# Optimization experiments

Hardware: AMD Instinct MI355X
Metric: run time of the kernel (lower is better)

The kernel has to match this reference:

```python
import jax, jax.numpy as jnp
import numpy as np

B, L, LQ = 64, 4096, 128
D = 32        # input_dim (value channels)
ET = 128      # embed_time
NH = 1        # num_heads
H = 128       # nhidden
NC = 6        # n_classes


def _time_emb(tt, lin_w, lin_b, per_w, per_b):
    # tt [..., T] -> [..., T, ET]; cat(Linear(1,1)(t), sin(Linear(1,ET-1)(t)))
    tt = tt[..., None]
    out1 = tt * lin_w[0, 0] + lin_b
    out2 = jnp.sin(tt @ per_w + per_b)
    return jnp.concatenate([out1, out2], axis=-1)


def _gru_dir(xs, wih, whh, bih, bhh, reverse):
    # xs [B, T, I] -> [B, T, H]; torch GRU gate math
    xs_t = jnp.swapaxes(xs, 0, 1)              # [T, B, I]
    if reverse:
        xs_t = xs_t[::-1]
    gi_all = xs_t @ wih.T + bih                # [T, B, 3H] precomputed input gates
    h0 = jnp.zeros((xs.shape[0], H), xs.dtype)

    def step(h, gi):
        gh = h @ whh.T + bhh
        ir, iz, inn = jnp.split(gi, 3, axis=-1)
        hr, hz, hn = jnp.split(gh, 3, axis=-1)
        r = jax.nn.sigmoid(ir + hr)
        z = jax.nn.sigmoid(iz + hz)
        n = jnp.tanh(inn + r * hn)
        h_new = (1.0 - z) * n + z * h
        return h_new, h_new

    _, ys = jax.lax.scan(step, h0, gi_all)     # [T, B, H]
    if reverse:
        ys = ys[::-1]
    return jnp.swapaxes(ys, 0, 1)


def _bigru(xs, wih, whh, bih, bhh):
    fwd = _gru_dir(xs, wih[0], whh[0], bih[0], bhh[0], False)
    bwd = _gru_dir(xs, wih[1], whh[1], bih[1], bhh[1], True)
    return jnp.concatenate([fwd, bwd], axis=-1)


def setup_inputs() -> dict:
    ks = jax.random.split(jax.random.key(0), 32)
    w = lambda i, s: jax.random.normal(ks[i], s, jnp.float32) * 0.05
    G3 = 3 * H
    return {
        "x": jax.random.normal(ks[0], (B, L, D), jnp.float32),
        "time_steps": jax.random.uniform(ks[1], (B, L), dtype=jnp.float32),
        "query_times": jnp.linspace(0.0, 1.0, LQ, dtype=jnp.float32),
        "lin_w": w(2, (1, 1)), "lin_b": w(3, (1,)),
        "per_w": w(4, (1, ET - 1)), "per_b": w(5, (ET - 1,)),
        "wq": w(6, (ET, ET)), "bq": w(7, (ET,)),
        "wk": w(8, (ET, ET)), "bk": w(9, (ET,)),
        "wo": w(10, (NH * D, H)), "bo": w(11, (H,)),
        "gru0_wih": w(12, (2, G3, H)), "gru0_whh": w(13, (2, G3, H)),
        "gru0_bih": w(14, (2, G3)), "gru0_bhh": w(15, (2, G3)),
        "gru1_wih": w(16, (2, G3, 2 * H)), "gru1_whh": w(17, (2, G3, H)),
        "gru1_bih": w(18, (2, G3)), "gru1_bhh": w(19, (2, G3)),
        "c1_w": w(20, (2 * H, 128)), "c1_b": w(21, (128,)),
        "c2_w": w(22, (128, 64)), "c2_b": w(23, (64,)),
        "c3_w": w(24, (64, NC)), "c3_b": w(25, (NC,)),
    }


def reference(x, time_steps, query_times, lin_w, lin_b, per_w, per_b,
              wq, bq, wk, bk, wo, bo,
              gru0_wih, gru0_whh, gru0_bih, gru0_bhh,
              gru1_wih, gru1_whh, gru1_bih, gru1_bhh,
              c1_w, c1_b, c2_w, c2_b, c3_w, c3_b):
    ek = ET // NH
    # learned time embeddings
    q = _time_emb(query_times[None, :], lin_w, lin_b, per_w, per_b)  # [1, LQ, ET]
    k = _time_emb(time_steps, lin_w, lin_b, per_w, per_b)            # [B, L, ET]
    # per-head projections
    qp = (q @ wq + bq).reshape(1, LQ, NH, ek).transpose(0, 2, 1, 3)[0]  # [NH, LQ, ek]
    kp = (k @ wk + bk).reshape(B, L, NH, ek).transpose(0, 2, 1, 3)      # [B, NH, L, ek]
    # mTAN attention: scores are channel-independent (mask=None), so the
    # per-channel repeat+softmax reduces to a single softmax over keys.
    scores = jnp.einsum('hqe,bhke->bhqk', qp, kp) / jnp.sqrt(jnp.float32(ek))
    p = jax.nn.softmax(scores, axis=-1)                                 # [B, NH, LQ, L]
    att = jnp.einsum('bhqk,bkd->bqhd', p, x).reshape(B, LQ, NH * D)
    att_out = att @ wo + bo                                             # [B, LQ, H]
    # 2-layer bidirectional GRU
    g0 = _bigru(att_out, gru0_wih, gru0_whh, gru0_bih, gru0_bhh)        # [B, LQ, 2H]
    g1 = _bigru(g0, gru1_wih, gru1_whh, gru1_bih, gru1_bhh)             # [B, LQ, 2H]
    class_in = jnp.concatenate([g1[:, -1, :H], g1[:, 0, H:]], axis=1)   # [B, 2H]
    out = ((class_in @ c1_w + c1_b) @ c2_w + c2_b) @ c3_w + c3_b        # [B, NC]
    return out
```

## Files before the change

### kernel.cpp

```cpp
#include <hip/hip_runtime.h>
#include <math.h>

#define Bn   64
#define Ln   4096
#define LQn  128
#define Dn   32
#define ETn  128
#define Hn   128
#define G3n  384
#define NDEG 12

typedef __attribute__((ext_vector_type(2))) float f32x2;

#define DPPF(x, ctrl) __int_as_float(__builtin_amdgcn_update_dpp(0, __float_as_int(x), (ctrl), 0xF, 0xF, true))
#define QP_XOR1 0xB1
#define QP_XOR2 0x4E
#define QP_B0   0x00
#define QP_B1   0x55
#define QP_B2   0xAA
#define QP_B3   0xFF

__device__ __forceinline__ float sin_poly(float x) {
    const float x2 = x * x;
    float r = -1.9841270114e-04f;
    r = fmaf(r, x2,  8.3333337680e-03f);
    r = fmaf(r, x2, -1.6666667163e-01f);
    return fmaf(r * x2, x, x);
}
__device__ __forceinline__ float cos_poly(float x) {
    const float x2 = x * x;
    float r =  2.4801587642e-05f;
    r = fmaf(r, x2, -1.3888888899e-03f);
    r = fmaf(r, x2,  4.1666667908e-02f);
    r = fmaf(r, x2, -5.0000000000e-01f);
    return fmaf(r, x2, 1.0f);
}

#define WS_C    0
#define WS_WT   4096
#define WS_B2   (WS_WT + 768*32)
#define WS_CLS  (WS_B2 + 1024)
#define WS_G0   (WS_CLS + Bn*2*Hn)
#define WS_GI   (WS_G0 + Bn*LQn*2*Hn)
#define WS_QPB  WS_G0
#define WS_BAS  (WS_G0 + 16384)
#define WS_ACCP WS_G0
#define WS_SP   (WS_G0 + 1048576)

__global__ __launch_bounds__(128) void k_basis(
    const float* __restrict__ per_w, const float* __restrict__ per_b,
    float* __restrict__ basis)
{
    const int j = threadIdx.x;
    if (j >= ETn - 1) return;
    const float w = per_w[j], b = per_b[j];
    const float sb = sin_poly(b), cb = cos_poly(b);
    float wp = 1.f;
#pragma unroll
    for (int d = 0; d < NDEG; ++d) {
        const float sd = ((d & 3) == 0) ? sb : ((d & 3) == 1) ? cb : ((d & 3) == 2) ? -sb : -cb;
        basis[d * 128 + j] = wp * sd;
        wp *= w / (float)(d + 1);
    }
}

__global__ __launch_bounds__(128) void k_qp(
    const float* __restrict__ qtimes, const float* __restrict__ lin_w,
    const float* __restrict__ lin_b, const float* __restrict__ per_w,
    const float* __restrict__ per_b, const float* __restrict__ wq,
    const float* __restrict__ bq, float* __restrict__ qp)
{
    __shared__ float qe[ETn];
    const int q = blockIdx.x, e = threadIdx.x;
    const float t = qtimes[q];
    qe[e] = (e == 0) ? fmaf(t, lin_w[0], lin_b[0])
                     : sin_poly(fmaf(t, per_w[e - 1], per_b[e - 1]));
    __syncthreads();
    float a = bq[e];
#pragma unroll 16
    for (int i = 0; i < ETn; ++i) a = fmaf(qe[i], wq[i * ETn + e], a);
    qp[q * ETn + e] = a;
}

__global__ __launch_bounds__(128) void k_qtc(
    const float* __restrict__ qp, const float* __restrict__ wk,
    const float* __restrict__ bk, const float* __restrict__ lin_w,
    const float* __restrict__ lin_b, const float* __restrict__ basis,
    float* __restrict__ C)
{
    __shared__ float qp_l[ETn], qt_l[ETn], red[96], qbk_red[32];
    const int q = blockIdx.x, tid = threadIdx.x;
    qp_l[tid] = qp[q * ETn + tid];
    __syncthreads();
    {
        const float4* wk4 = (const float4*)(wk + (size_t)tid * ETn);
        const float4* qp4 = (const float4*)qp_l;
        float a = 0.f;
#pragma unroll
        for (int k = 0; k < 32; ++k) {
            const float4 w4 = wk4[k], p4 = qp4[k];
            a += w4.x * p4.x + w4.y * p4.y + w4.z * p4.z + w4.w * p4.w;
        }
        qt_l[tid] = a;
    }
    __syncthreads();
    if (tid < 96) {
        const int d = tid >> 3, g = tid & 7;
        float p = 0.f;
        for (int j = g; j < ETn - 1; j += 8) p = fmaf(qt_l[j + 1], basis[d * 128 + j], p);
        red[tid] = p;
    } else {
        const int g2 = tid - 96;
        float p = 0.f;
#pragma unroll
        for (int k = 0; k < 4; ++k) p = fmaf(qp_l[g2 + 32 * k], bk[g2 + 32 * k], p);
        qbk_red[g2] = p;
    }
    __syncthreads();
    if (tid < NDEG) {
        const int d = tid;
        float s = red[d * 8 + 0] + red[d * 8 + 1] + red[d * 8 + 2] + red[d * 8 + 3]
                + red[d * 8 + 4] + red[d * 8 + 5] + red[d * 8 + 6] + red[d * 8 + 7];
        if (d == 0) {
            float qbk = 0.f;
#pragma unroll
            for (int k = 0; k < 32; ++k) qbk += qbk_red[k];
            s += qt_l[0] * lin_b[0] + qbk;
        }
        if (d == 1) s += qt_l[0] * lin_w[0];
        C[q * NDEG + d] = s * 0.08838834764831845f;
    }
}

__global__ __launch_bounds__(256) void k_fuse(
    const float* __restrict__ wih, const float* __restrict__ wo,
    const float* __restrict__ bo, const float* __restrict__ bih,
    float* __restrict__ Wt, float* __restrict__ bias2)
{
    const int t = blockIdx.x * 256 + threadIdx.x;
    if (t < 768 * 32) {
        const int o = t >> 5, d = t & 31;
        const float* wr = wih + (size_t)o * 128;
        const float* wc = wo + (size_t)d * 128;
        float a = 0.f;
        for (int h = 0; h < 128; ++h) a += wr[h] * wc[h];
        Wt[t] = a;
    } else if (t < 768 * 33) {
        const int o = t - 768 * 32;
        const float* wr = wih + (size_t)o * 128;
        float a = bih[o];
        for (int h = 0; h < 128; ++h) a += bo[h] * wr[h];
        bias2[o] = a;
    }
}

#define ACC8(m, pv) \
    acc[m][0].x = fmaf(pv, xa.x, acc[m][0].x); acc[m][0].y = fmaf(pv, xa.y, acc[m][0].y); \
    acc[m][0].z = fmaf(pv, xa.z, acc[m][0].z); acc[m][0].w = fmaf(pv, xa.w, acc[m][0].w); \
    acc[m][1].x = fmaf(pv, xb.x, acc[m][1].x); acc[m][1].y = fmaf(pv, xb.y, acc[m][1].y); \
    acc[m][1].z = fmaf(pv, xb.z, acc[m][1].z); acc[m][1].w = fmaf(pv, xb.w, acc[m][1].w);

__global__ __launch_bounds__(512, 2) void k_attn(
    const float* __restrict__ x, const float* __restrict__ tsteps,
    const float* __restrict__ Cc, float* __restrict__ accP, float* __restrict__ sP)
{
    __shared__ float slab[4][128][36];
    const int tid = threadIdx.x;
    const int b = blockIdx.x >> 2, lsplit = blockIdx.x & 3;
    const int i = tid & 3, qt = (tid >> 2) & 31, ls2 = tid >> 7;
    const int qown = 4 * qt + i;

    float c[NDEG];
#pragma unroll
    for (int d = 0; d < NDEG; ++d) c[d] = Cc[qown * NDEG + d];

    const int l0 = lsplit * 1024 + ls2 * 256;
    const float4* tg4 = (const float4*)(tsteps + (size_t)b * Ln + l0);
    const float4* xg  = (const float4*)(x + ((size_t)b * Ln + l0) * Dn);

    float4 acc[4][2];
#pragma unroll
    for (int m = 0; m < 4; ++m)
#pragma unroll
        for (int e = 0; e < 2; ++e) { acc[m][e].x = 0.f; acc[m][e].y = 0.f; acc[m][e].z = 0.f; acc[m][e].w = 0.f; }
    float s_own = 0.f;

    for (int k = 0; k < 64; ++k) {
        const float4 t4 = tg4[k];
#pragma unroll
        for (int jj = 0; jj < 4; ++jj) {
            const float t = (jj == 0) ? t4.x : (jj == 1) ? t4.y : (jj == 2) ? t4.z : t4.w;
            float sc = c[NDEG - 1];
#pragma unroll
            for (int d = NDEG - 2; d >= 0; --d) sc = fmaf(sc, t, c[d]);
            const float pe = __expf(sc);
            s_own += pe;
            const float p0 = DPPF(pe, QP_B0);
            const float p1 = DPPF(pe, QP_B1);
            const float p2 = DPPF(pe, QP_B2);
            const float p3 = DPPF(pe, QP_B3);
            const int lrow = (k * 4 + jj) * 8;
            const float4 xa = xg[lrow + 2 * i];
            const float4 xb = xg[lrow + 2 * i + 1];
            ACC8(0, p0) ACC8(1, p1) ACC8(2, p2) ACC8(3, p3)
        }
    }
#pragma unroll
    for (int m = 0; m < 4; ++m) {
        *(float4*)&slab[ls2][4 * qt + m][8 * i]     = acc[m][0];
        *(float4*)&slab[ls2][4 * qt + m][8 * i + 4] = acc[m][1];
    }
    slab[ls2][qown][32] = s_own;
    __syncthreads();
    const int q = tid & 127, part = tid >> 7;
#pragma unroll
    for (int j = 0; j < 2; ++j) {
        const int off = (part * 2 + j) * 4;
        float4 r  = *(float4*)&slab[0][q][off];
        float4 r1 = *(float4*)&slab[1][q][off];
        float4 r2 = *(float4*)&slab[2][q][off];
        float4 r3 = *(float4*)&slab[3][q][off];
        r.x += r1.x + r2.x + r3.x; r.y += r1.y + r2.y + r3.y;
        r.z += r1.z + r2.z + r3.z; r.w += r1.w + r2.w + r3.w;
        *(float4*)&accP[((((size_t)lsplit * Bn + b) * LQn + q) * 32) + off] = r;
    }
    if (part == 0) {
        sP[((size_t)lsplit * Bn + b) * LQn + q] =
            slab[0][q][32] + slab[1][q][32] + slab[2][q][32] + slab[3][q][32];
    }
}

__global__ __launch_bounds__(256) void k_gemm_att(
    const float* __restrict__ accP, const float* __restrict__ sP,
    const float* __restrict__ Bm, const float* __restrict__ bias,
    float* __restrict__ Cm)
{
    __shared__ float4 A_l[64 * 8];
    __shared__ float4 B_l[64 * 8];
    const int tid = threadIdx.x;
    const int m0 = blockIdx.x * 64, n0 = blockIdx.y * 64;
    const int r0 = (tid >> 4) << 2, c0 = (tid & 15) << 2;
    float acc[4][4] = {};
    const float4* Ag = (const float4*)accP;
    const float4* Bg = (const float4*)Bm;

#pragma unroll
    for (int w = 0; w < 2; ++w) {
        const int idx = tid + w * 256;
        const int row = idx >> 3, c4 = idx & 7;
        const int sc = (c4 + row + (row >> 2)) & 7;
        const int m = m0 + row;
        float4 a0 = Ag[(size_t)m * 8 + c4];
        float4 a1 = Ag[((size_t)8192  + m) * 8 + c4];
        float4 a2 = Ag[((size_t)16384 + m) * 8 + c4];
        float4 a3 = Ag[((size_t)24576 + m) * 8 + c4];
        const float inv = 1.f / (sP[m] + sP[8192 + m] + sP[16384 + m] + sP[24576 + m]);
        float4 av;
        av.x = (a0.x + a1.x + a2.x + a3.x) * inv;
        av.y = (a0.y + a1.y + a2.y + a3.y) * inv;
        av.z = (a0.z + a1.z + a2.z + a3.z) * inv;
        av.w = (a0.w + a1.w + a2.w + a3.w) * inv;
        A_l[row * 8 + sc] = av;
        B_l[row * 8 + sc] = Bg[(size_t)(n0 + row) * 8 + c4];
    }
    __syncthreads();
#pragma unroll
    for (int k4 = 0; k4 < 8; ++k4) {
        float4 av[4], bv[4];
#pragma unroll
        for (int j = 0; j < 4; ++j) {
            const int ra = r0 + j;
            av[j] = A_l[ra * 8 + ((k4 + ra + (ra >> 2)) & 7)];
        }
#pragma unroll
        for (int j = 0; j < 4; ++j) {
            const int rb = c0 + j;
            bv[j] = B_l[rb * 8 + ((k4 + rb + (rb >> 2)) & 7)];
        }
#pragma unroll
        for (int ri = 0; ri < 4; ++ri)
#pragma unroll
            for (int ci = 0; ci < 4; ++ci)
                acc[ri][ci] += av[ri].x * bv[ci].x + av[ri].y * bv[ci].y
                             + av[ri].z * bv[ci].z + av[ri].w * bv[ci].w;
    }
#pragma unroll
    for (int ri = 0; ri < 4; ++ri) {
        float4 o4;
        o4.x = acc[ri][0] + bias[n0 + c0 + 0];
        o4.y = acc[ri][1] + bias[n0 + c0 + 1];
        o4.z = acc[ri][2] + bias[n0 + c0 + 2];
        o4.w = acc[ri][3] + bias[n0 + c0 + 3];
        *(float4*)&Cm[(size_t)(m0 + r0 + ri) * 768 + n0 + c0] = o4;
    }
}

__global__ __launch_bounds__(256) void k_gemm_nt(
    const float* __restrict__ A, const float* __restrict__ Bm,
    const float* __restrict__ bias, float* __restrict__ Cm,
    int N, int K)
{
    __shared__ float4 A_l[64 * 8];
    __shared__ float4 B_l[64 * 8];
    const int tid = threadIdx.x;
    const int m0 = blockIdx.x * 64, n0 = blockIdx.y * 64;
    const int r0 = (tid >> 4) << 2, c0 = (tid & 15) << 2;
    const int K4 = K >> 2;
    float acc[4][4] = {};
    const float4* Ag = (const float4*)A;
    const float4* Bg = (const float4*)Bm;

    for (int k0 = 0; k0 < K4; k0 += 8) {
        __syncthreads();
#pragma unroll
        for (int w = 0; w < 2; ++w) {
            const int idx = tid + w * 256;
            const int row = idx >> 3, c4 = idx & 7;
            const int sc = (c4 + row + (row >> 2)) & 7;
            A_l[row * 8 + sc] = Ag[(size_t)(m0 + row) * K4 + k0 + c4];
            B_l[row * 8 + sc] = Bg[(size_t)(n0 + row) * K4 + k0 + c4];
        }
        __syncthreads();
#pragma unroll
        for (int k4 = 0; k4 < 8; ++k4) {
            float4 av[4], bv[4];
#pragma unroll
            for (int j = 0; j < 4; ++j) {
                const int ra = r0 + j;
                av[j] = A_l[ra * 8 + ((k4 + ra + (ra >> 2)) & 7)];
            }
#pragma unroll
            for (int j = 0; j < 4; ++j) {
                const int rb = c0 + j;
                bv[j] = B_l[rb * 8 + ((k4 + rb + (rb >> 2)) & 7)];
            }
#pragma unroll
            for (int ri = 0; ri < 4; ++ri)
#pragma unroll
                for (int ci = 0; ci < 4; ++ci)
                    acc[ri][ci] += av[ri].x * bv[ci].x + av[ri].y * bv[ci].y
                                 + av[ri].z * bv[ci].z + av[ri].w * bv[ci].w;
        }
    }
#pragma unroll
    for (int ri = 0; ri < 4; ++ri) {
        float4 o4;
        o4.x = acc[ri][0] + bias[n0 + c0 + 0];
        o4.y = acc[ri][1] + bias[n0 + c0 + 1];
        o4.z = acc[ri][2] + bias[n0 + c0 + 2];
        o4.w = acc[ri][3] + bias[n0 + c0 + 3];
        *(float4*)&Cm[(size_t)(m0 + r0 + ri) * N + n0 + c0] = o4;
    }
}

__global__ __launch_bounds__(256, 1) void k_gru(
    const float* __restrict__ gi, const float* __restrict__ whh,
    const float* __restrict__ bhh, float* __restrict__ seq_out,
    float* __restrict__ final_out)
{
    __shared__ float h_l[2][Hn];
    const int tid = threadIdx.x;
    const int b = blockIdx.x >> 1, dir = blockIdx.x & 1;
    const int j = tid >> 1, q = tid & 1;

    f32x2 wr[32], wz[32], wn[32];
    {
        const float* wb = whh + ((size_t)dir * G3n + j) * Hn + 64 * q;
        const f32x2* p0 = (const f32x2*)(wb);
        const f32x2* p1 = (const f32x2*)(wb + (size_t)128 * Hn);
        const f32x2* p2 = (const f32x2*)(wb + (size_t)256 * Hn);
#pragma unroll
        for (int k = 0; k < 32; ++k) { wr[k] = p0[k]; wz[k] = p1[k]; wn[k] = p2[k]; }
    }
#pragma unroll
    for (int k = 0; k < 32; ++k) {
        asm volatile("" : "+v"(wr[k]));
        asm volatile("" : "+v"(wz[k]));
        asm volatile("" : "+v"(wn[k]));
    }
    const float bhr = bhh[dir * G3n + j];
    const float bhz = bhh[dir * G3n + 128 + j];
    const float bhn = bhh[dir * G3n + 256 + j];

    if (tid < Hn) { h_l[0][tid] = 0.f; h_l[1][tid] = 0.f; }
    __syncthreads();

    const long sstride = dir ? -768 : 768;
    const float* gptr = gi + (size_t)b * LQn * 768 + dir * G3n + j
                        + (size_t)(dir ? LQn - 1 : 0) * 768;

    int cur = 0;
    float hlast = 0.f;

    auto gstep = [&](const float gir, const float giz, const float gin,
                     const int step) {
        const float hold = h_l[cur][j];
        const float4* hb = (const float4*)(&h_l[cur][q * 64]);
        f32x2 ar = {0.f, 0.f}, az = {0.f, 0.f}, an = {0.f, 0.f};
        f32x2 br = {0.f, 0.f}, bz = {0.f, 0.f}, bn = {0.f, 0.f};
#pragma unroll
        for (int cc = 0; cc < 16; ++cc) {
            float4 hv = hb[cc];
            f32x2 h01; h01.x = hv.x; h01.y = hv.y;
            f32x2 h23; h23.x = hv.z; h23.y = hv.w;
            asm("v_pk_fma_f32 %0, %1, %2, %0" : "+v"(ar) : "v"(wr[2 * cc]),     "v"(h01));
            asm("v_pk_fma_f32 %0, %1, %2, %0" : "+v"(az) : "v"(wz[2 * cc]),     "v"(h01));
            asm("v_pk_fma_f32 %0, %1, %2, %0" : "+v"(an) : "v"(wn[2 * cc]),     "v"(h01));
            asm("v_pk_fma_f32 %0, %1, %2, %0" : "+v"(br) : "v"(wr[2 * cc + 1]), "v"(h23));
            asm("v_pk_fma_f32 %0, %1, %2, %0" : "+v"(bz) : "v"(wz[2 * cc + 1]), "v"(h23));
            asm("v_pk_fma_f32 %0, %1, %2, %0" : "+v"(bn) : "v"(wn[2 * cc + 1]), "v"(h23));
        }
        float sr = (ar.x + br.x) + (ar.y + br.y);
        float sz = (az.x + bz.x) + (az.y + bz.y);
        float sn = (an.x + bn.x) + (an.y + bn.y);
        sr += DPPF(sr, QP_XOR1);
        sz += DPPF(sz, QP_XOR1);
        sn += DPPF(sn, QP_XOR1);
        const float r = 1.f / (1.f + __expf(-(gir + sr + bhr)));
        const float z = 1.f / (1.f + __expf(-(giz + sz + bhz)));
        const float nx = gin + r * (sn + bhn);
        const float n = 1.f - 2.f / (1.f + __expf(2.f * nx));
        const float hn = n + z * (hold - n);
        if (q == 0) {
            h_l[cur ^ 1][j] = hn;
            if (seq_out) {
                const int l = dir ? (LQn - 1 - step) : step;
                seq_out[((size_t)(b * LQn + l)) * (2 * Hn) + dir * Hn + j] = hn;
            }
        }
        hlast = hn;
        cur ^= 1;
        __syncthreads();
    };

    float gA[3], gB[3], gC[3], gD[3];
#define GLD(dst, s) { const long o = (long)(s) * sstride; \
    dst[0] = gptr[o]; dst[1] = gptr[o + 128]; dst[2] = gptr[o + 256]; }
    GLD(gA, 0) GLD(gB, 1) GLD(gC, 2) GLD(gD, 3)
    for (int s0 = 0; s0 < LQn; s0 += 4) {
        gstep(gA[0], gA[1], gA[2], s0);
        { const int sn2 = (s0 + 4 < LQn) ? s0 + 4 : LQn - 1; GLD(gA, sn2) }
        gstep(gB[0], gB[1], gB[2], s0 + 1);
        { const int sn2 = (s0 + 5 < LQn) ? s0 + 5 : LQn - 1; GLD(gB, sn2) }
        gstep(gC[0], gC[1], gC[2], s0 + 2);
        { const int sn2 = (s0 + 6 < LQn) ? s0 + 6 : LQn - 1; GLD(gC, sn2) }
        gstep(gD[0], gD[1], gD[2], s0 + 3);
        { const int sn2 = (s0 + 7 < LQn) ? s0 + 7 : LQn - 1; GLD(gD, sn2) }
    }
#undef GLD
    if (final_out && q == 0) final_out[b * 2 * Hn + dir * Hn + j] = hlast;
}

__global__ __launch_bounds__(256) void k_cls(
    const float* __restrict__ cls_in,
    const float* __restrict__ c1w, const float* __restrict__ c1b,
    const float* __restrict__ c2w, const float* __restrict__ c2b,
    const float* __restrict__ c3w, const float* __restrict__ c3b,
    float* __restrict__ out)
{
    __shared__ float ci[256], y1[128], y2[64];
    const int b = blockIdx.x, tid = threadIdx.x;
    ci[tid] = cls_in[b * 256 + tid];
    __syncthreads();
    if (tid < 128) { float a = c1b[tid]; for (int i = 0; i < 256; ++i) a += ci[i] * c1w[i * 128 + tid]; y1[tid] = a; }
    __syncthreads();
    if (tid < 64)  { float a = c2b[tid]; for (int i = 0; i < 128; ++i) a += y1[i] * c2w[i * 64 + tid];  y2[tid] = a; }
    __syncthreads();
    if (tid < 6)   { float a = c3b[tid]; for (int i = 0; i < 64; ++i)  a += y2[i] * c3w[i * 6 + tid];   out[b * 6 + tid] = a; }
}

extern "C" void kernel_launch(void* const* d_in, const int* in_sizes, int n_in,
                              void* d_out, int out_size, void* d_ws, size_t ws_size,
                              hipStream_t stream)
{
    const float* x        = (const float*)d_in[0];
    const float* tsteps   = (const float*)d_in[1];
    const float* qtimes   = (const float*)d_in[2];
    const float* lin_w    = (const float*)d_in[3];
    const float* lin_b    = (const float*)d_in[4];
    const float* per_w    = (const float*)d_in[5];
    const float* per_b    = (const float*)d_in[6];
    const float* wq       = (const float*)d_in[7];
    const float* bq       = (const float*)d_in[8];
    const float* wk       = (const float*)d_in[9];
    const float* bk       = (const float*)d_in[10];
    const float* wo       = (const float*)d_in[11];
    const float* bo       = (const float*)d_in[12];
    const float* g0_wih   = (const float*)d_in[13];
    const float* g0_whh   = (const float*)d_in[14];
    const float* g0_bih   = (const float*)d_in[15];
    const float* g0_bhh   = (const float*)d_in[16];
    const float* g1_wih   = (const float*)d_in[17];
    const float* g1_whh   = (const float*)d_in[18];
    const float* g1_bih   = (const float*)d_in[19];
    const float* g1_bhh   = (const float*)d_in[20];
    const float* c1w      = (const float*)d_in[21];
    const float* c1b      = (const float*)d_in[22];
    const float* c2w      = (const float*)d_in[23];
    const float* c2b      = (const float*)d_in[24];
    const float* c3w      = (const float*)d_in[25];
    const float* c3b      = (const float*)d_in[26];
    float* out = (float*)d_out;
    float* ws  = (float*)d_ws;

    float* Cws   = ws + WS_C;
    float* Wt    = ws + WS_WT;
    float* bias2 = ws + WS_B2;
    float* clsin = ws + WS_CLS;
    float* g0buf = ws + WS_G0;
    float* qpB   = ws + WS_QPB;
    float* basB  = ws + WS_BAS;
    float* accP  = ws + WS_ACCP;
    float* sPb   = ws + WS_SP;
    float* gibuf = ws + WS_GI;

    k_basis<<<1, 128, 0, stream>>>(per_w, per_b, basB);
    k_qp<<<128, 128, 0, stream>>>(qtimes, lin_w, lin_b, per_w, per_b, wq, bq, qpB);
    k_qtc<<<128, 128, 0, stream>>>(qpB, wk, bk, lin_w, lin_b, basB, Cws);

    k_fuse<<<99, 256, 0, stream>>>(g0_wih, wo, bo, g0_bih, Wt, bias2);
    k_attn<<<256, 512, 0, stream>>>(x, tsteps, Cws, accP, sPb);

    k_gemm_att<<<dim3(128, 12), 256, 0, stream>>>(accP, sPb, Wt, bias2, gibuf);
    k_gru<<<128, 256, 0, stream>>>(gibuf, g0_whh, g0_bhh, g0buf, nullptr);

    k_gemm_nt<<<dim3(128, 12), 256, 0, stream>>>(g0buf, g1_wih, g1_bih, gibuf, 768, 256);
    k_gru<<<128, 256, 0, stream>>>(gibuf, g1_whh, g1_bhh, nullptr, clsin);

    k_cls<<<64, 256, 0, stream>>>(clsin, c1w, c1b, c2w, c2b, c3w, c3b, out);
}
```

Before: 326.5 us.

## Fuse coefficient kernels, stage x through LDS in attention, use packed FMA

Merges the basis, query-projection and coefficient kernels into one launch, so two launches and the global round-trips between them go away. The attention kernel now stages x chunks through shared memory with register prefetch, drops to one block per CU, and accumulates with packed two-wide FMAs. Both GEMM kernels switch to packed f32x2 FMA accumulators, k_fuse uses float4 loads, and the GRU drops its asm register pins. These changes add extra barriers and lower attention occupancy, and removing the pins may let the compiler spill or reload the GRU weights.

```diff
diff --git a/kernel.cpp b/kernel.cpp
--- a/kernel.cpp
+++ b/kernel.cpp
@@ -42,55 +42,39 @@
 #define WS_CLS  (WS_B2 + 1024)
 #define WS_G0   (WS_CLS + Bn*2*Hn)
 #define WS_GI   (WS_G0 + Bn*LQn*2*Hn)
-#define WS_QPB  WS_G0
-#define WS_BAS  (WS_G0 + 16384)
 #define WS_ACCP WS_G0
 #define WS_SP   (WS_G0 + 1048576)
 
-__global__ __launch_bounds__(128) void k_basis(
-    const float* __restrict__ per_w, const float* __restrict__ per_b,
-    float* __restrict__ basis)
-{
-    const int j = threadIdx.x;
-    if (j >= ETn - 1) return;
-    const float w = per_w[j], b = per_b[j];
-    const float sb = sin_poly(b), cb = cos_poly(b);
-    float wp = 1.f;
-#pragma unroll
-    for (int d = 0; d < NDEG; ++d) {
-        const float sd = ((d & 3) == 0) ? sb : ((d & 3) == 1) ? cb : ((d & 3) == 2) ? -sb : -cb;
-        basis[d * 128 + j] = wp * sd;
-        wp *= w / (float)(d + 1);
-    }
-}
-
-__global__ __launch_bounds__(128) void k_qp(
+__global__ __launch_bounds__(128) void k_coef(
     const float* __restrict__ qtimes, const float* __restrict__ lin_w,
     const float* __restrict__ lin_b, const float* __restrict__ per_w,
     const float* __restrict__ per_b, const float* __restrict__ wq,
-    const float* __restrict__ bq, float* __restrict__ qp)
-{
-    __shared__ float qe[ETn];
-    const int q = blockIdx.x, e = threadIdx.x;
+    const float* __restrict__ bq, const float* __restrict__ wk,
+    const float* __restrict__ bk, float* __restrict__ C)
+{
+    __shared__ float qe[ETn], qp_l[ETn], qt_l[ETn], bas[NDEG * 128], red[96], qbk_red[32];
+    const int q = blockIdx.x, tid = threadIdx.x;
+    if (tid < ETn - 1) {
+        const float w = per_w[tid], bb = per_b[tid];
+        const float sb = sin_poly(bb), cb = cos_poly(bb);
+        float wp = 1.f;
+#pragma unroll
+        for (int d = 0; d < NDEG; ++d) {
+            const float sd = ((d & 3) == 0) ? sb : ((d & 3) == 1) ? cb : ((d & 3) == 2) ? -sb : -cb;
+            bas[d * 128 + tid] = wp * sd;
+            wp *= w / (float)(d + 1);
+        }
+    }
     const float t = qtimes[q];
-    qe[e] = (e == 0) ? fmaf(t, lin_w[0], lin_b[0])
-                     : sin_poly(fmaf(t, per_w[e - 1], per_b[e - 1]));
-    __syncthreads();
-    float a = bq[e];
+    qe[tid] = (tid == 0) ? fmaf(t, lin_w[0], lin_b[0])
+                         : sin_poly(fmaf(t, per_w[tid - 1], per_b[tid - 1]));
+    __syncthreads();
+    {
+        float a = bq[tid];
 #pragma unroll 16
-    for (int i = 0; i < ETn; ++i) a = fmaf(qe[i], wq[i * ETn + e], a);
-    qp[q * ETn + e] = a;
-}
-
-__global__ __launch_bounds__(128) void k_qtc(
-    const float* __restrict__ qp, const float* __restrict__ wk,
-    const float* __restrict__ bk, const float* __restrict__ lin_w,
-    const float* __restrict__ lin_b, const float* __restrict__ basis,
-    float* __restrict__ C)
-{
-    __shared__ float qp_l[ETn], qt_l[ETn], red[96], qbk_red[32];
-    const int q = blockIdx.x, tid = threadIdx.x;
-    qp_l[tid] = qp[q * ETn + tid];
+        for (int i = 0; i < ETn; ++i) a = fmaf(qe[i], wq[i * ETn + tid], a);
+        qp_l[tid] = a;
+    }
     __syncthreads();
     {
         const float4* wk4 = (const float4*)(wk + (size_t)tid * ETn);
@@ -107,7 +91,7 @@
     if (tid < 96) {
         const int d = tid >> 3, g = tid & 7;
         float p = 0.f;
-        for (int j = g; j < ETn - 1; j += 8) p = fmaf(qt_l[j + 1], basis[d * 128 + j], p);
+        for (int j = g; j < ETn - 1; j += 8) p = fmaf(qt_l[j + 1], bas[d * 128 + j], p);
         red[tid] = p;
     } else {
         const int g2 = tid - 96;
@@ -140,35 +124,40 @@
     const int t = blockIdx.x * 256 + threadIdx.x;
     if (t < 768 * 32) {
         const int o = t >> 5, d = t & 31;
-        const float* wr = wih + (size_t)o * 128;
-        const float* wc = wo + (size_t)d * 128;
+        const float4* wr4 = (const float4*)(wih + (size_t)o * 128);
+        const float4* wc4 = (const float4*)(wo + (size_t)d * 128);
         float a = 0.f;
-        for (int h = 0; h < 128; ++h) a += wr[h] * wc[h];
+#pragma unroll
+        for (int k = 0; k < 32; ++k) {
+            const float4 r4 = wr4[k], c4 = wc4[k];
+            a += r4.x * c4.x + r4.y * c4.y + r4.z * c4.z + r4.w * c4.w;
+        }
         Wt[t] = a;
     } else if (t < 768 * 33) {
         const int o = t - 768 * 32;
-        const float* wr = wih + (size_t)o * 128;
+        const float4* wr4 = (const float4*)(wih + (size_t)o * 128);
+        const float4* bo4 = (const float4*)bo;
         float a = bih[o];
-        for (int h = 0; h < 128; ++h) a += bo[h] * wr[h];
+#pragma unroll
+        for (int k = 0; k < 32; ++k) {
+            const float4 r4 = wr4[k], b4 = bo4[k];
+            a += r4.x * b4.x + r4.y * b4.y + r4.z * b4.z + r4.w * b4.w;
+        }
         bias2[o] = a;
     }
 }
 
-#define ACC8(m, pv) \
-    acc[m][0].x = fmaf(pv, xa.x, acc[m][0].x); acc[m][0].y = fmaf(pv, xa.y, acc[m][0].y); \
-    acc[m][0].z = fmaf(pv, xa.z, acc[m][0].z); acc[m][0].w = fmaf(pv, xa.w, acc[m][0].w); \
-    acc[m][1].x = fmaf(pv, xb.x, acc[m][1].x); acc[m][1].y = fmaf(pv, xb.y, acc[m][1].y); \
-    acc[m][1].z = fmaf(pv, xb.z, acc[m][1].z); acc[m][1].w = fmaf(pv, xb.w, acc[m][1].w);
-
-__global__ __launch_bounds__(512, 2) void k_attn(
+__global__ __launch_bounds__(512, 1) void k_attn(
     const float* __restrict__ x, const float* __restrict__ tsteps,
     const float* __restrict__ Cc, float* __restrict__ accP, float* __restrict__ sP)
 {
-    __shared__ float slab[4][128][36];
+    __shared__ float4 xls[4 * 64 * 8];
+    __shared__ float  slab[4][128][36];
     const int tid = threadIdx.x;
     const int b = blockIdx.x >> 2, lsplit = blockIdx.x & 3;
     const int i = tid & 3, qt = (tid >> 2) & 31, ls2 = tid >> 7;
     const int qown = 4 * qt + i;
+    const int u = tid & 127;
 
     float c[NDEG];
 #pragma unroll
@@ -178,37 +167,67 @@
     const float4* tg4 = (const float4*)(tsteps + (size_t)b * Ln + l0);
     const float4* xg  = (const float4*)(x + ((size_t)b * Ln + l0) * Dn);
 
-    float4 acc[4][2];
+    f32x2 acc2[4][4];
 #pragma unroll
     for (int m = 0; m < 4; ++m)
 #pragma unroll
-        for (int e = 0; e < 2; ++e) { acc[m][e].x = 0.f; acc[m][e].y = 0.f; acc[m][e].z = 0.f; acc[m][e].w = 0.f; }
+        for (int e = 0; e < 4; ++e) { acc2[m][e].x = 0.f; acc2[m][e].y = 0.f; }
     float s_own = 0.f;
 
-    for (int k = 0; k < 64; ++k) {
-        const float4 t4 = tg4[k];
-#pragma unroll
-        for (int jj = 0; jj < 4; ++jj) {
-            const float t = (jj == 0) ? t4.x : (jj == 1) ? t4.y : (jj == 2) ? t4.z : t4.w;
-            float sc = c[NDEG - 1];
-#pragma unroll
-            for (int d = NDEG - 2; d >= 0; --d) sc = fmaf(sc, t, c[d]);
-            const float pe = __expf(sc);
-            s_own += pe;
-            const float p0 = DPPF(pe, QP_B0);
-            const float p1 = DPPF(pe, QP_B1);
-            const float p2 = DPPF(pe, QP_B2);
-            const float p3 = DPPF(pe, QP_B3);
-            const int lrow = (k * 4 + jj) * 8;
-            const float4 xa = xg[lrow + 2 * i];
-            const float4 xb = xg[lrow + 2 * i + 1];
-            ACC8(0, p0) ACC8(1, p1) ACC8(2, p2) ACC8(3, p3)
-        }
-    }
+    float4 xr[4];
+#pragma unroll
+    for (int w = 0; w < 4; ++w) xr[w] = xg[u + 128 * w];
+
+    for (int ch = 0; ch < 4; ++ch) {
+        __syncthreads();
+#pragma unroll
+        for (int w = 0; w < 4; ++w) xls[ls2 * 512 + u + 128 * w] = xr[w];
+        __syncthreads();
+        if (ch < 3) {
+            const int off = (ch + 1) * 512;
+#pragma unroll
+            for (int w = 0; w < 4; ++w) xr[w] = xg[off + u + 128 * w];
+        }
+        const float4* xrow = &xls[ls2 * 512];
+        for (int k = 0; k < 16; ++k) {
+            const float4 t4 = tg4[ch * 16 + k];
+#pragma unroll
+            for (int jj = 0; jj < 4; ++jj) {
+                const float t = (jj == 0) ? t4.x : (jj == 1) ? t4.y : (jj == 2) ? t4.z : t4.w;
+                float sc = c[NDEG - 1];
+#pragma unroll
+                for (int d = NDEG - 2; d >= 0; --d) sc = fmaf(sc, t, c[d]);
+                const float pe = __expf(sc);
+                s_own += pe;
+                const float p0 = DPPF(pe, QP_B0);
+                const float p1 = DPPF(pe, QP_B1);
+                const float p2 = DPPF(pe, QP_B2);
+                const float p3 = DPPF(pe, QP_B3);
+                const int lrow = (k * 4 + jj) * 8;
+                const float4 xa = xrow[lrow + 2 * i];
+                const float4 xb = xrow[lrow + 2 * i + 1];
+                f32x2 xa0; xa0.x = xa.x; xa0.y = xa.y;
+                f32x2 xa1; xa1.x = xa.z; xa1.y = xa.w;
+                f32x2 xb0; xb0.x = xb.x; xb0.y = xb.y;
+                f32x2 xb1; xb1.x = xb.z; xb1.y = xb.w;
+#define PKA(m, pv) { f32x2 pp; pp.x = (pv); pp.y = (pv); \
+    acc2[m][0] = __builtin_elementwise_fma(pp, xa0, acc2[m][0]); \
+    acc2[m][1] = __builtin_elementwise_fma(pp, xa1, acc2[m][1]); \
+    acc2[m][2] = __builtin_elementwise_fma(pp, xb0, acc2[m][2]); \
+    acc2[m][3] = __builtin_elementwise_fma(pp, xb1, acc2[m][3]); }
+                PKA(0, p0) PKA(1, p1) PKA(2, p2) PKA(3, p3)
+#undef PKA
+            }
+        }
+    }
+    __syncthreads();
 #pragma unroll
     for (int m = 0; m < 4; ++m) {
-        *(float4*)&slab[ls2][4 * qt + m][8 * i]     = acc[m][0];
-        *(float4*)&slab[ls2][4 * qt + m][8 * i + 4] = acc[m][1];
+        float4 f4a, f4b;
+        f4a.x = acc2[m][0].x; f4a.y = acc2[m][0].y; f4a.z = acc2[m][1].x; f4a.w = acc2[m][1].y;
+        f4b.x = acc2[m][2].x; f4b.y = acc2[m][2].y; f4b.z = acc2[m][3].x; f4b.w = acc2[m][3].y;
+        *(float4*)&slab[ls2][4 * qt + m][8 * i]     = f4a;
+        *(float4*)&slab[ls2][4 * qt + m][8 * i + 4] = f4b;
     }
     slab[ls2][qown][32] = s_own;
     __syncthreads();
@@ -240,7 +259,11 @@
     const int tid = threadIdx.x;
     const int m0 = blockIdx.x * 64, n0 = blockIdx.y * 64;
     const int r0 = (tid >> 4) << 2, c0 = (tid & 15) << 2;
-    float acc[4][4] = {};
+    f32x2 acc2[4][4];
+#pragma unroll
+    for (int a = 0; a < 4; ++a)
+#pragma unroll
+        for (int bb = 0; bb < 4; ++bb) { acc2[a][bb].x = 0.f; acc2[a][bb].y = 0.f; }
     const float4* Ag = (const float4*)accP;
     const float4* Bg = (const float4*)Bm;
 
@@ -278,19 +301,25 @@
             bv[j] = B_l[rb * 8 + ((k4 + rb + (rb >> 2)) & 7)];
         }
 #pragma unroll
-        for (int ri = 0; ri < 4; ++ri)
-#pragma unroll
-            for (int ci = 0; ci < 4; ++ci)
-                acc[ri][ci] += av[ri].x * bv[ci].x + av[ri].y * bv[ci].y
-                             + av[ri].z * bv[ci].z + av[ri].w * bv[ci].w;
+        for (int ri = 0; ri < 4; ++ri) {
+            f32x2 alo; alo.x = av[ri].x; alo.y = av[ri].y;
+            f32x2 ahi; ahi.x = av[ri].z; ahi.y = av[ri].w;
+#pragma unroll
+            for (int ci = 0; ci < 4; ++ci) {
+                f32x2 blo; blo.x = bv[ci].x; blo.y = bv[ci].y;
+                f32x2 bhi; bhi.x = bv[ci].z; bhi.y = bv[ci].w;
+                acc2[ri][ci] = __builtin_elementwise_fma(alo, blo, acc2[ri][ci]);
+                acc2[ri][ci] = __builtin_elementwise_fma(ahi, bhi, acc2[ri][ci]);
+            }
+        }
     }
 #pragma unroll
     for (int ri = 0; ri < 4; ++ri) {
         float4 o4;
-        o4.x = acc[ri][0] + bias[n0 + c0 + 0];
-        o4.y = acc[ri][1] + bias[n0 + c0 + 1];
-        o4.z = acc[ri][2] + bias[n0 + c0 + 2];
-        o4.w = acc[ri][3] + bias[n0 + c0 + 3];
+        o4.x = acc2[ri][0].x + acc2[ri][0].y + bias[n0 + c0 + 0];
+        o4.y = acc2[ri][1].x + acc2[ri][1].y + bias[n0 + c0 + 1];
+        o4.z = acc2[ri][2].x + acc2[ri][2].y + bias[n0 + c0 + 2];
+        o4.w = acc2[ri][3].x + acc2[ri][3].y + bias[n0 + c0 + 3];
         *(float4*)&Cm[(size_t)(m0 + r0 + ri) * 768 + n0 + c0] = o4;
     }
 }
@@ -306,7 +335,11 @@
     const int m0 = blockIdx.x * 64, n0 = blockIdx.y * 64;
     const int r0 = (tid >> 4) << 2, c0 = (tid & 15) << 2;
     const int K4 = K >> 2;
-    float acc[4][4] = {};
+    f32x2 acc2[4][4];
+#pragma unroll
+    for (int a = 0; a < 4; ++a)
+#pragma unroll
+        for (int bb = 0; bb < 4; ++bb) { acc2[a][bb].x = 0.f; acc2[a][bb].y = 0.f; }
     const float4* Ag = (const float4*)A;
     const float4* Bg = (const float4*)Bm;
 
@@ -335,20 +368,26 @@
                 bv[j] = B_l[rb * 8 + ((k4 + rb + (rb >> 2)) & 7)];
             }
 #pragma unroll
-            for (int ri = 0; ri < 4; ++ri)
-#pragma unroll
-                for (int ci = 0; ci < 4; ++ci)
-                    acc[ri][ci] += av[ri].x * bv[ci].x + av[ri].y * bv[ci].y
-                                 + av[ri].z * bv[ci].z + av[ri].w * bv[ci].w;
+            for (int ri = 0; ri < 4; ++ri) {
+                f32x2 alo; alo.x = av[ri].x; alo.y = av[ri].y;
+                f32x2 ahi; ahi.x = av[ri].z; ahi.y = av[ri].w;
+#pragma unroll
+                for (int ci = 0; ci < 4; ++ci) {
+                    f32x2 blo; blo.x = bv[ci].x; blo.y = bv[ci].y;
+                    f32x2 bhi; bhi.x = bv[ci].z; bhi.y = bv[ci].w;
+                    acc2[ri][ci] = __builtin_elementwise_fma(alo, blo, acc2[ri][ci]);
+                    acc2[ri][ci] = __builtin_elementwise_fma(ahi, bhi, acc2[ri][ci]);
+                }
+            }
         }
     }
 #pragma unroll
     for (int ri = 0; ri < 4; ++ri) {
         float4 o4;
-        o4.x = acc[ri][0] + bias[n0 + c0 + 0];
-        o4.y = acc[ri][1] + bias[n0 + c0 + 1];
-        o4.z = acc[ri][2] + bias[n0 + c0 + 2];
-        o4.w = acc[ri][3] + bias[n0 + c0 + 3];
+        o4.x = acc2[ri][0].x + acc2[ri][0].y + bias[n0 + c0 + 0];
+        o4.y = acc2[ri][1].x + acc2[ri][1].y + bias[n0 + c0 + 1];
+        o4.z = acc2[ri][2].x + acc2[ri][2].y + bias[n0 + c0 + 2];
+        o4.w = acc2[ri][3].x + acc2[ri][3].y + bias[n0 + c0 + 3];
         *(float4*)&Cm[(size_t)(m0 + r0 + ri) * N + n0 + c0] = o4;
     }
 }
@@ -371,12 +410,6 @@
         const f32x2* p2 = (const f32x2*)(wb + (size_t)256 * Hn);
 #pragma unroll
         for (int k = 0; k < 32; ++k) { wr[k] = p0[k]; wz[k] = p1[k]; wn[k] = p2[k]; }
-    }
-#pragma unroll
-    for (int k = 0; k < 32; ++k) {
-        asm volatile("" : "+v"(wr[k]));
-        asm volatile("" : "+v"(wz[k]));
-        asm volatile("" : "+v"(wn[k]));
     }
     const float bhr = bhh[dir * G3n + j];
     const float bhz = bhh[dir * G3n + 128 + j];
@@ -508,16 +541,11 @@
     float* bias2 = ws + WS_B2;
     float* clsin = ws + WS_CLS;
     float* g0buf = ws + WS_G0;
-    float* qpB   = ws + WS_QPB;
-    float* basB  = ws + WS_BAS;
     float* accP  = ws + WS_ACCP;
     float* sPb   = ws + WS_SP;
     float* gibuf = ws + WS_GI;
 
-    k_basis<<<1, 128, 0, stream>>>(per_w, per_b, basB);
-    k_qp<<<128, 128, 0, stream>>>(qtimes, lin_w, lin_b, per_w, per_b, wq, bq, qpB);
-    k_qtc<<<128, 128, 0, stream>>>(qpB, wk, bk, lin_w, lin_b, basB, Cws);
-
+    k_coef<<<128, 128, 0, stream>>>(qtimes, lin_w, lin_b, per_w, per_b, wq, bq, wk, bk, Cws);
     k_fuse<<<99, 256, 0, stream>>>(g0_wih, wo, bo, g0_bih, Wt, bias2);
     k_attn<<<256, 512, 0, stream>>>(x, tsteps, Cws, accP, sPb);
 
```

Result: no change. 325.2 us (-0.4%).
